# Performance work log

Hardware: AMD Instinct MI355X
Metric: run time of the kernel (lower is better)

## Reference

```python
import jax, jax.numpy as jnp
import numpy as np

N_NODES = 10000
N_EDGES = 100000
D_IN = 2 * 1280   # concat of row/col node embeddings
H1 = 512
H2 = 256


def gcn_conv(x, edge_index, W, b):
    """PyG GCNConv: add self-loops, symmetric deg^-1/2 normalization,
    x @ W then scatter-add of normalized messages, plus bias.
    num_nodes is inferred from x.shape[0] (here = n_edges, faithful to source)."""
    N = x.shape[0]
    loops = jnp.arange(N, dtype=edge_index.dtype)
    row = jnp.concatenate([edge_index[0], loops])  # sources
    col = jnp.concatenate([edge_index[1], loops])  # targets
    deg = jax.ops.segment_sum(jnp.ones_like(row, dtype=x.dtype), col, num_segments=N)
    dinv = jax.lax.rsqrt(deg)  # deg >= 1 thanks to self-loops
    norm = dinv[row] * dinv[col]  # [E+N]
    h = x @ W  # [N, out]
    out = jax.ops.segment_sum(h[row] * norm[:, None], col, num_segments=N)
    return out + b


def setup_inputs() -> dict:
    key = jax.random.key(0)
    ks = jax.random.split(key, 9)
    x = jax.random.normal(ks[0], (N_NODES, 1280), dtype=jnp.float32)
    edge_index = jax.random.randint(ks[1], (2, N_EDGES), 0, N_NODES, dtype=jnp.int32)
    # uniform noise for gumbel-sigmoid (torch.rand); keep strictly in (0,1)
    eps = jax.random.uniform(ks[2], (N_EDGES, 1), jnp.float32, 1e-6, 1.0 - 1e-6)
    W1 = jax.random.normal(ks[3], (D_IN, H1), jnp.float32) * (1.0 / np.sqrt(D_IN))
    b1 = jnp.zeros((H1,), jnp.float32)
    W2 = jax.random.normal(ks[4], (H1, H2), jnp.float32) * (1.0 / np.sqrt(H1))
    b2 = jnp.zeros((H2,), jnp.float32)
    Wl = jax.random.normal(ks[5], (H2, 1), jnp.float32) * (1.0 / np.sqrt(H2))
    bl = jnp.zeros((1,), jnp.float32)
    return {"x": x, "edge_index": edge_index, "eps": eps,
            "W1": W1, "b1": b1, "W2": W2, "b2": b2, "Wl": Wl, "bl": bl}


def reference(x, edge_index, eps, W1, b1, W2, b2, Wl, bl):
    rows, cols = edge_index[0], edge_index[1]
    # per-edge explainer input: concat of endpoint embeddings -> [E, 2560]
    input_embs = jnp.concatenate([x[rows], x[cols]], axis=1)
    h = jax.nn.relu(gcn_conv(input_embs, edge_index, W1, b1))
    h = jax.nn.relu(gcn_conv(h, edge_index, W2, b2))
    pre = h @ Wl + bl  # [E, 1] sampling weights
    # gumbel-sigmoid sampling (temperature = 1.0)
    gate = jnp.log(eps) - jnp.log1p(-eps) + pre
    mask = jax.nn.sigmoid(gate)
    pos, neg = mask, 1.0 - mask
    kld = jnp.mean(pos * jnp.log(pos / 0.5 + 1e-8) + neg * jnp.log(neg / 0.5 + 1e-9))
    return (kld, mask)
```

## Files before the change

### kernel.cpp

```cpp
#include <hip/hip_runtime.h>
#include <cstdint>
#include <cstddef>

#define H1DIM 512
#define H2DIM 256
#define DNODE 1280
#define NPACK 1024

typedef __attribute__((ext_vector_type(8))) short short8v;
typedef __attribute__((ext_vector_type(4))) float f32x4;
typedef __attribute__((ext_vector_type(4))) unsigned short us4;

__device__ __forceinline__ unsigned short f2bf(float f) {
    unsigned int u = __builtin_bit_cast(unsigned int, f);
    u += 0x7fffu + ((u >> 16) & 1u);
    return (unsigned short)(u >> 16);
}
__device__ __forceinline__ float bf2f(unsigned short h) {
    unsigned int u = ((unsigned int)h) << 16;
    return __builtin_bit_cast(float, u);
}

__device__ __forceinline__ int cmi(int R, int kq) {
    return ((R >> 4) << 9) + (((kq >> 3) << 4) + (R & 15)) * 8;
}

__global__ __launch_bounds__(256) void prep_k(
    const float* __restrict__ x, unsigned short* __restrict__ xb, int ncvt, int ntot,
    const int* __restrict__ e1, int* __restrict__ hist, int nhist, int E,
    const float* __restrict__ W1, unsigned short* __restrict__ Bpt1,
    const float* __restrict__ W2, unsigned short* __restrict__ W2t)
{
    __shared__ float tile[32][33];
    int b = blockIdx.x;

    if (b < ncvt) {
        int i = b * 256 + threadIdx.x;
        if (i * 4 < ntot) {
            f32x4 v = *reinterpret_cast<const f32x4*>(x + (size_t)i * 4);
            us4 o;
            o[0] = f2bf(v.x); o[1] = f2bf(v.y); o[2] = f2bf(v.z); o[3] = f2bf(v.w);
            *reinterpret_cast<us4*>(xb + (size_t)i * 4) = o;
        }
        return;
    }
    b -= ncvt;
    if (b < nhist) {
        int e = b * 256 + threadIdx.x;
        if (e < E) atomicAdd(&hist[e1[e]], 1);
        return;
    }
    b -= nhist;

    const float* src; unsigned short* dst; int ldsrc, lddst, bx, by;
    if (b < 640) {
        src = W1; dst = Bpt1; ldsrc = H1DIM; lddst = DNODE; bx = b & 15; by = b >> 4;
    } else if (b < 1280) {
        b -= 640;
        src = W1 + (size_t)DNODE * H1DIM; dst = Bpt1 + (size_t)H1DIM * DNODE;
        ldsrc = H1DIM; lddst = DNODE; bx = b & 15; by = b >> 4;
    } else {
        b -= 1280;
        src = W2; dst = W2t; ldsrc = H2DIM; lddst = H1DIM; bx = b & 7; by = b >> 3;
    }
    const int c0 = bx * 32, r0 = by * 32;
    const int tx = threadIdx.x & 31;
    const int ty = threadIdx.x >> 5;
#pragma unroll
    for (int rr = ty; rr < 32; rr += 8)
        tile[rr][tx] = src[(size_t)(r0 + rr) * ldsrc + c0 + tx];
    __syncthreads();
#pragma unroll
    for (int rr = ty; rr < 32; rr += 8)
        dst[(size_t)(c0 + rr) * lddst + r0 + tx] = f2bf(tile[tx][rr]);
}

template <int MODE>
__global__ __launch_bounds__(512) void gemm_u_k(
    const unsigned short* __restrict__ Ab,
    const unsigned short* __restrict__ Bt,
    unsigned short* __restrict__ Cb,
    const unsigned short* __restrict__ out1b,
    const unsigned short* __restrict__ XWb16,
    const float* __restrict__ b1,
    const float* __restrict__ b2,
    const float* __restrict__ Wl,
    const int* __restrict__ e0, const int* __restrict__ e1,
    unsigned short* __restrict__ h2b, float* __restrict__ pre_raw,
    int* __restrict__ hist, int* __restrict__ off, int* __restrict__ cursor,
    float* __restrict__ dinv,
    int M, int K, int Nn, int nwg)
{
    const int tid  = threadIdx.x;

    if (MODE == 0 && blockIdx.x >= nwg) {
        __shared__ int part[512];
        const int t = tid;
        const int per = (Nn + 511) / 512;
        const int base = t * per;
        int s = 0;
        for (int i = 0; i < per; ++i) { int b = base + i; if (b < Nn) s += hist[b]; }
        part[t] = s;
        __syncthreads();
        for (int d = 1; d < 512; d <<= 1) {
            int v = (t >= d) ? part[t - d] : 0;
            __syncthreads();
            part[t] += v;
            __syncthreads();
        }
        int run = (t == 0) ? 0 : part[t - 1];
        for (int i = 0; i < per; ++i) {
            int b = base + i;
            if (b < Nn) {
                int h = hist[b];
                off[b] = run;
                run += h;
                cursor[b] = 0;
                dinv[b] = rsqrtf(1.0f + (float)h);
            }
        }
        if (t == 511) off[Nn] = run;
        return;
    }

    __shared__ alignas(16) unsigned short As[2][128 * 32];
    __shared__ alignas(16) unsigned short Bs[2][256 * 32];
    __shared__ float b1s[H1DIM];
    __shared__ float b2s[H2DIM];
    __shared__ float wls[H2DIM];
    __shared__ float preacc[128];

    const int lane = tid & 63;
    const int w    = tid >> 6;
    const int wm   = w >> 2, wn = w & 3;

    int mb, n0;
    if (MODE == 0) {
        const int q = nwg >> 3, r = nwg & 7;
        const int xcd = blockIdx.x & 7;
        const int base = (xcd < r) ? xcd * (q + 1) : r * (q + 1) + (xcd - r) * q;
        const int wg = base + (blockIdx.x >> 3);
        mb = wg >> 2;
        n0 = (wg & 3) << 8;
    } else {
        mb = blockIdx.x;
        n0 = 0;
    }
    const int m0 = mb * 128;

    if (MODE == 1) {
        if (tid < 128) preacc[tid] = 0.f;
        if (tid < 256) { b2s[tid] = b2[tid]; wls[tid] = Wl[tid]; }
        b1s[tid] = b1[tid];
    }

    const int sa_r = tid >> 2, sa_k = (tid & 3) << 3;
    const int sb_r = tid >> 1, sb_k = (tid & 1) << 4;
    const int gma  = m0 + sa_r;
    const bool aval = (gma < M);

    const int aw  = cmi(sa_r, sa_k);
    const int bw0 = cmi(sb_r, sb_k);
    const int bw1 = cmi(sb_r, sb_k + 8);

    const unsigned short* bsrc = Bt + (size_t)(n0 + sb_r) * K + sb_k;
    const unsigned short* s1 = nullptr;
    const unsigned short* s2 = nullptr;
    bool dual = false;
    if (MODE == 0) {
        if (aval) s1 = Ab + (size_t)gma * K + sa_k;
    } else if (aval) {
        if (gma < Nn) {
            s1 = out1b + (size_t)gma * H1DIM + sa_k;
        } else {
            s1 = XWb16 + (size_t)e0[gma] * NPACK + sa_k;
            s2 = XWb16 + (size_t)e1[gma] * NPACK + H1DIM + sa_k;
            dual = true;
        }
    }
    if (MODE == 1) __syncthreads();

    f32x4 acc[4][4];
#pragma unroll
    for (int i = 0; i < 4; ++i)
#pragma unroll
        for (int j = 0; j < 4; ++j) acc[i][j] = f32x4{0.f, 0.f, 0.f, 0.f};

    short8v ab1, ab2, bb0, bb1;

    auto load_tile = [&](int k0) {
        bb0 = *reinterpret_cast<const short8v*>(bsrc + k0);
        bb1 = *reinterpret_cast<const short8v*>(bsrc + k0 + 8);
        if (aval) {
            ab1 = *reinterpret_cast<const short8v*>(s1 + k0);
            if (MODE == 1 && dual) ab2 = *reinterpret_cast<const short8v*>(s2 + k0);
        }
    };
    auto write_lds = [&](int buf, int k0) {
        *reinterpret_cast<short8v*>(&Bs[buf][bw0]) = bb0;
        *reinterpret_cast<short8v*>(&Bs[buf][bw1]) = bb1;
        short8v av;
        if (!aval) {
            av = short8v{0,0,0,0,0,0,0,0};
        } else if (MODE == 0 || !dual) {
            av = ab1;
        } else {
#pragma unroll
            for (int ii = 0; ii < 8; ++ii) {
                float v = bf2f((unsigned short)ab1[ii]) + bf2f((unsigned short)ab2[ii])
                        + b1s[k0 + sa_k + ii];
                v = fmaxf(v, 0.f);
                av[ii] = (short)f2bf(v);
            }
        }
        *reinterpret_cast<short8v*>(&As[buf][aw]) = av;
    };

    load_tile(0);
    int buf = 0;
    for (int k0 = 0; k0 < K; k0 += 32) {
        write_lds(buf, k0);
        __syncthreads();
        if (k0 + 32 < K) load_tile(k0 + 32);

        const unsigned short* ard = &As[buf][(wm * 4) * 512 + lane * 8];
        const unsigned short* brd = &Bs[buf][(wn * 4) * 512 + lane * 8];
        short8v af[4], bfq[4];
#pragma unroll
        for (int i = 0; i < 4; ++i)
            af[i] = *reinterpret_cast<const short8v*>(ard + i * 512);
#pragma unroll
        for (int j = 0; j < 4; ++j)
            bfq[j] = *reinterpret_cast<const short8v*>(brd + j * 512);
#pragma unroll
        for (int i = 0; i < 4; ++i)
#pragma unroll
            for (int j = 0; j < 4; ++j)
                acc[i][j] = __builtin_amdgcn_mfma_f32_16x16x32_bf16(af[i], bfq[j], acc[i][j], 0, 0, 0);
        buf ^= 1;
    }

    const int crow0 = m0 + wm * 64 + ((lane >> 4) << 2);
    if (MODE == 0) {
        const int ccol = n0 + wn * 64 + (lane & 15);
#pragma unroll
        for (int i = 0; i < 4; ++i)
#pragma unroll
            for (int q = 0; q < 4; ++q) {
                const int row = crow0 + i * 16 + q;
                if (row < M) {
#pragma unroll
                    for (int j = 0; j < 4; ++j)
                        Cb[(size_t)row * NPACK + ccol + j * 16] = f2bf(acc[i][j][q]);
                }
            }
    } else {
        const int cbase = wn * 64 + (lane & 15);
#pragma unroll
        for (int i = 0; i < 4; ++i)
#pragma unroll
            for (int q = 0; q < 4; ++q) {
                float v = 0.f;
#pragma unroll
                for (int j = 0; j < 4; ++j) {
                    const int c = cbase + j * 16;
                    v += fmaxf(acc[i][j][q] + b2s[c], 0.f) * wls[c];
                }
                v += __shfl_xor(v, 1, 64);
                v += __shfl_xor(v, 2, 64);
                v += __shfl_xor(v, 4, 64);
                v += __shfl_xor(v, 8, 64);
                if ((lane & 15) == 0)
                    atomicAdd(&preacc[wm * 64 + i * 16 + ((lane >> 4) << 2) + q], v);
            }
        if (m0 < Nn) {
            const int ccol = wn * 64 + (lane & 15);
#pragma unroll
            for (int i = 0; i < 4; ++i)
#pragma unroll
                for (int q = 0; q < 4; ++q) {
                    const int row = crow0 + i * 16 + q;
                    if (row < Nn) {
#pragma unroll
                        for (int j = 0; j < 4; ++j)
                            h2b[(size_t)row * H2DIM + ccol + j * 16] = f2bf(acc[i][j][q]);
                    }
                }
        }
        __syncthreads();
        if (tid < 128) {
            const int gm = m0 + tid;
            if (gm >= Nn && gm < M) pre_raw[gm] = preacc[tid];
        }
    }
}

__global__ __launch_bounds__(256) void build1_fill_k(
    const unsigned short* __restrict__ XWb16, const float* __restrict__ dinv,
    const int* __restrict__ e0, const int* __restrict__ e1,
    unsigned short* __restrict__ H1b,
    const int* __restrict__ off, int* __restrict__ cursor, int* __restrict__ srcs,
    int N, int E)
{
    int b = blockIdx.x;
    if (b < N) {
        const int a = e0[b], c = e1[b];
        const float dv = dinv[b];
        const unsigned short* pt = XWb16 + (size_t)a * NPACK;
        const unsigned short* pb = XWb16 + (size_t)c * NPACK + H1DIM;
        const int j = threadIdx.x * 2;
        const unsigned ut = *reinterpret_cast<const unsigned*>(pt + j);
        const unsigned ub = *reinterpret_cast<const unsigned*>(pb + j);
        const float ox = (bf2f((unsigned short)(ut & 0xffff)) + bf2f((unsigned short)(ub & 0xffff))) * dv;
        const float oy = (bf2f((unsigned short)(ut >> 16))   + bf2f((unsigned short)(ub >> 16)))   * dv;
        const unsigned pk = (unsigned)f2bf(ox) | ((unsigned)f2bf(oy) << 16);
        *reinterpret_cast<unsigned*>(H1b + (size_t)b * H1DIM + j) = pk;
        return;
    }
    int e = (b - N) * 256 + threadIdx.x;
    if (e < E) {
        int t = e1[e];
        int p = off[t] + atomicAdd(&cursor[t], 1);
        srcs[p] = e0[e];
    }
}

__global__ __launch_bounds__(256) void agg1_k(
    const unsigned short* __restrict__ H1b, const int* __restrict__ off, const int* __restrict__ srcs,
    const float* __restrict__ b1, const float* __restrict__ dinv,
    unsigned short* __restrict__ out1b)
{
    const int t = blockIdx.x;
    const int j = threadIdx.x * 2;
    const int s0 = off[t], s1e = off[t + 1];
    const float dt = dinv[t];
    const unsigned u0 = *reinterpret_cast<const unsigned*>(H1b + (size_t)t * H1DIM + j);
    float ax = bf2f((unsigned short)(u0 & 0xffff));
    float ay = bf2f((unsigned short)(u0 >> 16));
    for (int i = s0; i < s1e; ++i) {
        const unsigned v = *reinterpret_cast<const unsigned*>(H1b + (size_t)srcs[i] * H1DIM + j);
        ax += bf2f((unsigned short)(v & 0xffff));
        ay += bf2f((unsigned short)(v >> 16));
    }
    const float ox = fmaxf(b1[j]     + dt * ax, 0.f);
    const float oy = fmaxf(b1[j + 1] + dt * ay, 0.f);
    const unsigned pk = (unsigned)f2bf(ox) | ((unsigned)f2bf(oy) << 16);
    *reinterpret_cast<unsigned*>(out1b + (size_t)t * H1DIM + j) = pk;
}

__global__ __launch_bounds__(128) void agg2_k(
    const unsigned short* __restrict__ h2b, const int* __restrict__ off, const int* __restrict__ srcs,
    const float* __restrict__ b2, const float* __restrict__ Wl,
    const float* __restrict__ dinv, float* __restrict__ pre_low)
{
    __shared__ float part[2];
    const int t = blockIdx.x;
    const int j = threadIdx.x * 2;
    const int s0 = off[t], s1e = off[t + 1];
    const float dt = dinv[t];
    const unsigned u0 = *reinterpret_cast<const unsigned*>(h2b + (size_t)t * H2DIM + j);
    float ax = bf2f((unsigned short)(u0 & 0xffff)) * dt;
    float ay = bf2f((unsigned short)(u0 >> 16)) * dt;
    for (int i = s0; i < s1e; ++i) {
        const int s = srcs[i];
        const float ds = dinv[s];
        const unsigned v = *reinterpret_cast<const unsigned*>(h2b + (size_t)s * H2DIM + j);
        ax += bf2f((unsigned short)(v & 0xffff)) * ds;
        ay += bf2f((unsigned short)(v >> 16)) * ds;
    }
    float p = fmaxf(b2[j]     + dt * ax, 0.f) * Wl[j]
            + fmaxf(b2[j + 1] + dt * ay, 0.f) * Wl[j + 1];
#pragma unroll
    for (int o = 32; o; o >>= 1) p += __shfl_down(p, o, 64);
    if ((threadIdx.x & 63) == 0) part[threadIdx.x >> 6] = p;
    __syncthreads();
    if (threadIdx.x == 0) pre_low[t] = part[0] + part[1];
}

__global__ __launch_bounds__(256) void final2_k(
    const float* __restrict__ pre_low, const float* __restrict__ pre_raw,
    const float* __restrict__ blp, const float* __restrict__ eps,
    float* __restrict__ dout, int E, int Nn)
{
    __shared__ float part[4];
    const int i = blockIdx.x * 256 + threadIdx.x;
    float kld = 0.f;
    if (i < E) {
        const float pre = ((i < Nn) ? pre_low[i] : pre_raw[i]) + blp[0];
        const float ee = eps[i];
        const float gate = logf(ee) - log1pf(-ee) + pre;
        const float m = 1.0f / (1.0f + expf(-gate));
        dout[1 + i] = m;
        const float pos = m, neg = 1.0f - m;
        kld = pos * logf(pos * 2.0f + 1e-8f) + neg * logf(neg * 2.0f + 1e-9f);
    }
#pragma unroll
    for (int o = 32; o; o >>= 1) kld += __shfl_down(kld, o, 64);
    const int lane = threadIdx.x & 63, wv = threadIdx.x >> 6;
    if (lane == 0) part[wv] = kld;
    __syncthreads();
    if (threadIdx.x == 0)
        atomicAdd(&dout[0], (part[0] + part[1] + part[2] + part[3]) / (float)E);
}

extern "C" void kernel_launch(void* const* d_in, const int* in_sizes, int n_in,
                              void* d_out, int out_size, void* d_ws, size_t ws_size,
                              hipStream_t stream)
{
    const float* x   = (const float*)d_in[0];
    const int*   ei  = (const int*)d_in[1];
    const float* eps = (const float*)d_in[2];
    const float* W1  = (const float*)d_in[3];
    const float* b1  = (const float*)d_in[4];
    const float* W2  = (const float*)d_in[5];
    const float* b2  = (const float*)d_in[6];
    const float* Wl  = (const float*)d_in[7];
    const float* bl  = (const float*)d_in[8];
    float* out = (float*)d_out;
    float* ws  = (float*)d_ws;

    const int N = in_sizes[0] / DNODE;
    const int E = in_sizes[1] / 2;
    const int* e0 = ei;
    const int* e1 = ei + E;

    float* dinv     = ws;
    float* pre_raw  = dinv + 16384;
    float* pre_low  = pre_raw + E;
    float* fend     = pre_low + 16384;
    unsigned short* XWb16 = (unsigned short*)fend;
    unsigned short* out1b = XWb16 + (size_t)N * NPACK;
    unsigned short* H1b   = out1b + (size_t)N * H1DIM;
    unsigned short* h2b   = H1b + (size_t)N * H1DIM;
    unsigned short* xb    = h2b + (size_t)N * H2DIM;
    unsigned short* Bpt1  = xb + (size_t)N * DNODE;
    unsigned short* W2t   = Bpt1 + (size_t)NPACK * DNODE;
    int* hist   = (int*)(W2t + (size_t)H2DIM * H1DIM);
    int* cursor = hist + N;
    int* off    = cursor + N;
    int* srcs   = off + (N + 1);

    hipMemsetAsync(hist, 0, (size_t)N * sizeof(int), stream);
    hipMemsetAsync(out, 0, sizeof(float), stream);

    {
        const int ntot = N * DNODE;
        const int ncvt = (ntot / 4 + 255) / 256;
        const int nhist = (E + 255) / 256;
        const int ntr = 640 + 640 + 128;
        prep_k<<<ncvt + nhist + ntr, 256, 0, stream>>>(
            x, xb, ncvt, ntot, e1, hist, nhist, E, W1, Bpt1, W2, W2t);
    }

    {
        const int nwg = 4 * ((N + 127) / 128);
        gemm_u_k<0><<<nwg + 1, 512, 0, stream>>>(
            xb, Bpt1, XWb16, nullptr, nullptr, b1, b2, Wl, e0, e1,
            nullptr, nullptr, hist, off, cursor, dinv, N, DNODE, N, nwg);
    }

    build1_fill_k<<<N + (E + 255) / 256, 256, 0, stream>>>(
        XWb16, dinv, e0, e1, H1b, off, cursor, srcs, N, E);

    agg1_k<<<N, 256, 0, stream>>>(H1b, off, srcs, b1, dinv, out1b);

    {
        const int nwg = (E + 127) / 128;
        gemm_u_k<1><<<nwg, 512, 0, stream>>>(
            nullptr, W2t, nullptr, out1b, XWb16, b1, b2, Wl, e0, e1,
            h2b, pre_raw, nullptr, nullptr, nullptr, nullptr, E, H1DIM, N, nwg);
    }

    agg2_k<<<N, 128, 0, stream>>>(h2b, off, srcs, b2, Wl, dinv, pre_low);

    final2_k<<<(E + 255) / 256, 256, 0, stream>>>(pre_low, pre_raw, bl, eps, out, E, N);
}
```

Baseline: 193.2 us.

## Fuse layer-1 aggregation into layer-2 GEMM with flag sync and fold final epilogue

Moves the agg1 neighbour aggregation into the front of the MODE 1 GEMM launch. Aggregation blocks each handle two nodes and bump a global release counter. GEMM tiles that need aggregated node rows (m0 < N) spin on that counter, while tiles over raw edge rows run first. The gumbel-sigmoid and KLD epilogue now runs inside the GEMM for rows at or above N and inside agg2 for rows below N, which removes final2_k and the pre_raw/pre_low buffers. This cuts two launches and some intermediate traffic, but the spin-wait relies on the aggregation blocks being scheduled before the waiting blocks, and it adds one atomic per node in agg2.

```diff
diff --git a/kernel.cpp b/kernel.cpp
--- a/kernel.cpp
+++ b/kernel.cpp
@@ -80,20 +80,23 @@
     const unsigned short* __restrict__ Ab,
     const unsigned short* __restrict__ Bt,
     unsigned short* __restrict__ Cb,
-    const unsigned short* __restrict__ out1b,
+    unsigned short* __restrict__ out1b,
     const unsigned short* __restrict__ XWb16,
+    const unsigned short* __restrict__ H1b,
     const float* __restrict__ b1,
     const float* __restrict__ b2,
     const float* __restrict__ Wl,
     const int* __restrict__ e0, const int* __restrict__ e1,
-    unsigned short* __restrict__ h2b, float* __restrict__ pre_raw,
-    int* __restrict__ hist, int* __restrict__ off, int* __restrict__ cursor,
-    float* __restrict__ dinv,
+    int* __restrict__ off, const int* __restrict__ srcs,
+    unsigned short* __restrict__ h2b,
+    int* __restrict__ hist, int* __restrict__ cursor, float* __restrict__ dinv,
+    const float* __restrict__ eps, const float* __restrict__ blp, float* __restrict__ dout,
+    int* __restrict__ flag, int nagg,
     int M, int K, int Nn, int nwg)
 {
     const int tid  = threadIdx.x;
 
-    if (MODE == 0 && blockIdx.x >= nwg) {
+    if (MODE == 0 && blockIdx.x >= (unsigned)nwg) {
         __shared__ int part[512];
         const int t = tid;
         const int per = (Nn + 511) / 512;
@@ -123,12 +126,38 @@
         return;
     }
 
+    if (MODE == 1 && blockIdx.x < (unsigned)nagg) {
+        const int t = ((int)blockIdx.x << 1) + (tid >> 8);
+        const int j = (tid & 255) << 1;
+        if (t < Nn) {
+            const int s0 = off[t], s1e = off[t + 1];
+            const float dt = dinv[t];
+            const unsigned u0 = *reinterpret_cast<const unsigned*>(H1b + (size_t)t * H1DIM + j);
+            float ax = bf2f((unsigned short)(u0 & 0xffff));
+            float ay = bf2f((unsigned short)(u0 >> 16));
+            for (int i = s0; i < s1e; ++i) {
+                const unsigned v = *reinterpret_cast<const unsigned*>(H1b + (size_t)srcs[i] * H1DIM + j);
+                ax += bf2f((unsigned short)(v & 0xffff));
+                ay += bf2f((unsigned short)(v >> 16));
+            }
+            const float ox = fmaxf(b1[j]     + dt * ax, 0.f);
+            const float oy = fmaxf(b1[j + 1] + dt * ay, 0.f);
+            const unsigned pk = (unsigned)f2bf(ox) | ((unsigned)f2bf(oy) << 16);
+            *reinterpret_cast<unsigned*>(out1b + (size_t)t * H1DIM + j) = pk;
+        }
+        __syncthreads();
+        if (tid == 0)
+            __hip_atomic_fetch_add(flag, 1, __ATOMIC_RELEASE, __HIP_MEMORY_SCOPE_AGENT);
+        return;
+    }
+
     __shared__ alignas(16) unsigned short As[2][128 * 32];
     __shared__ alignas(16) unsigned short Bs[2][256 * 32];
     __shared__ float b1s[H1DIM];
     __shared__ float b2s[H2DIM];
     __shared__ float wls[H2DIM];
     __shared__ float preacc[128];
+    __shared__ float kpart[8];
 
     const int lane = tid & 63;
     const int w    = tid >> 6;
@@ -143,8 +172,18 @@
         mb = wg >> 2;
         n0 = (wg & 3) << 8;
     } else {
-        mb = blockIdx.x;
+        const int ndep = (Nn + 127) >> 7;
+        const int b = (int)blockIdx.x - nagg;
+        const int ngat = nwg - ndep;
+        mb = (b < ngat) ? (ndep + b) : (b - ngat);
         n0 = 0;
+        if (mb < ndep) {
+            if (tid == 0) {
+                while (__hip_atomic_load(flag, __ATOMIC_ACQUIRE, __HIP_MEMORY_SCOPE_AGENT) < nagg)
+                    __builtin_amdgcn_s_sleep(8);
+            }
+            __syncthreads();
+        }
     }
     const int m0 = mb * 128;
 
@@ -288,9 +327,28 @@
                 }
         }
         __syncthreads();
+        float kld = 0.f;
         if (tid < 128) {
             const int gm = m0 + tid;
-            if (gm >= Nn && gm < M) pre_raw[gm] = preacc[tid];
+            if (gm >= Nn && gm < M) {
+                const float pre = preacc[tid] + blp[0];
+                const float ee = eps[gm];
+                const float gate = logf(ee) - log1pf(-ee) + pre;
+                const float mk = 1.0f / (1.0f + expf(-gate));
+                dout[1 + gm] = mk;
+                kld = mk * logf(mk * 2.0f + 1e-8f)
+                    + (1.0f - mk) * logf((1.0f - mk) * 2.0f + 1e-9f);
+            }
+        }
+#pragma unroll
+        for (int o = 32; o; o >>= 1) kld += __shfl_down(kld, o, 64);
+        if (lane == 0) kpart[w] = kld;
+        __syncthreads();
+        if (tid == 0) {
+            float s = 0.f;
+#pragma unroll
+            for (int i = 0; i < 8; ++i) s += kpart[i];
+            if (s != 0.f) atomicAdd(&dout[0], s / (float)M);
         }
     }
 }
@@ -325,33 +383,12 @@
     }
 }
 
-__global__ __launch_bounds__(256) void agg1_k(
-    const unsigned short* __restrict__ H1b, const int* __restrict__ off, const int* __restrict__ srcs,
-    const float* __restrict__ b1, const float* __restrict__ dinv,
-    unsigned short* __restrict__ out1b)
-{
-    const int t = blockIdx.x;
-    const int j = threadIdx.x * 2;
-    const int s0 = off[t], s1e = off[t + 1];
-    const float dt = dinv[t];
-    const unsigned u0 = *reinterpret_cast<const unsigned*>(H1b + (size_t)t * H1DIM + j);
-    float ax = bf2f((unsigned short)(u0 & 0xffff));
-    float ay = bf2f((unsigned short)(u0 >> 16));
-    for (int i = s0; i < s1e; ++i) {
-        const unsigned v = *reinterpret_cast<const unsigned*>(H1b + (size_t)srcs[i] * H1DIM + j);
-        ax += bf2f((unsigned short)(v & 0xffff));
-        ay += bf2f((unsigned short)(v >> 16));
-    }
-    const float ox = fmaxf(b1[j]     + dt * ax, 0.f);
-    const float oy = fmaxf(b1[j + 1] + dt * ay, 0.f);
-    const unsigned pk = (unsigned)f2bf(ox) | ((unsigned)f2bf(oy) << 16);
-    *reinterpret_cast<unsigned*>(out1b + (size_t)t * H1DIM + j) = pk;
-}
-
 __global__ __launch_bounds__(128) void agg2_k(
     const unsigned short* __restrict__ h2b, const int* __restrict__ off, const int* __restrict__ srcs,
     const float* __restrict__ b2, const float* __restrict__ Wl,
-    const float* __restrict__ dinv, float* __restrict__ pre_low)
+    const float* __restrict__ dinv,
+    const float* __restrict__ eps, const float* __restrict__ blp,
+    float* __restrict__ dout, int Etot)
 {
     __shared__ float part[2];
     const int t = blockIdx.x;
@@ -374,33 +411,16 @@
     for (int o = 32; o; o >>= 1) p += __shfl_down(p, o, 64);
     if ((threadIdx.x & 63) == 0) part[threadIdx.x >> 6] = p;
     __syncthreads();
-    if (threadIdx.x == 0) pre_low[t] = part[0] + part[1];
-}
-
-__global__ __launch_bounds__(256) void final2_k(
-    const float* __restrict__ pre_low, const float* __restrict__ pre_raw,
-    const float* __restrict__ blp, const float* __restrict__ eps,
-    float* __restrict__ dout, int E, int Nn)
-{
-    __shared__ float part[4];
-    const int i = blockIdx.x * 256 + threadIdx.x;
-    float kld = 0.f;
-    if (i < E) {
-        const float pre = ((i < Nn) ? pre_low[i] : pre_raw[i]) + blp[0];
-        const float ee = eps[i];
+    if (threadIdx.x == 0) {
+        const float pre = part[0] + part[1] + blp[0];
+        const float ee = eps[t];
         const float gate = logf(ee) - log1pf(-ee) + pre;
-        const float m = 1.0f / (1.0f + expf(-gate));
-        dout[1 + i] = m;
-        const float pos = m, neg = 1.0f - m;
-        kld = pos * logf(pos * 2.0f + 1e-8f) + neg * logf(neg * 2.0f + 1e-9f);
-    }
-#pragma unroll
-    for (int o = 32; o; o >>= 1) kld += __shfl_down(kld, o, 64);
-    const int lane = threadIdx.x & 63, wv = threadIdx.x >> 6;
-    if (lane == 0) part[wv] = kld;
-    __syncthreads();
-    if (threadIdx.x == 0)
-        atomicAdd(&dout[0], (part[0] + part[1] + part[2] + part[3]) / (float)E);
+        const float mk = 1.0f / (1.0f + expf(-gate));
+        dout[1 + t] = mk;
+        const float kld = mk * logf(mk * 2.0f + 1e-8f)
+                        + (1.0f - mk) * logf((1.0f - mk) * 2.0f + 1e-9f);
+        atomicAdd(&dout[0], kld / (float)Etot);
+    }
 }
 
 extern "C" void kernel_launch(void* const* d_in, const int* in_sizes, int n_in,
@@ -425,9 +445,7 @@
     const int* e1 = ei + E;
 
     float* dinv     = ws;
-    float* pre_raw  = dinv + 16384;
-    float* pre_low  = pre_raw + E;
-    float* fend     = pre_low + 16384;
+    float* fend     = dinv + 16384;
     unsigned short* XWb16 = (unsigned short*)fend;
     unsigned short* out1b = XWb16 + (size_t)N * NPACK;
     unsigned short* H1b   = out1b + (size_t)N * H1DIM;
@@ -436,12 +454,13 @@
     unsigned short* Bpt1  = xb + (size_t)N * DNODE;
     unsigned short* W2t   = Bpt1 + (size_t)NPACK * DNODE;
     int* hist   = (int*)(W2t + (size_t)H2DIM * H1DIM);
-    int* cursor = hist + N;
+    int* flag   = hist + N;
+    int* cursor = flag + 1;
     int* off    = cursor + N;
     int* srcs   = off + (N + 1);
 
-    hipMemsetAsync(hist, 0, (size_t)N * sizeof(int), stream);
-    hipMemsetAsync(out, 0, sizeof(float), stream);
+    (void)hipMemsetAsync(hist, 0, (size_t)(N + 1) * sizeof(int), stream);
+    (void)hipMemsetAsync(out, 0, sizeof(float), stream);
 
     {
         const int ntot = N * DNODE;
@@ -455,23 +474,22 @@
     {
         const int nwg = 4 * ((N + 127) / 128);
         gemm_u_k<0><<<nwg + 1, 512, 0, stream>>>(
-            xb, Bpt1, XWb16, nullptr, nullptr, b1, b2, Wl, e0, e1,
-            nullptr, nullptr, hist, off, cursor, dinv, N, DNODE, N, nwg);
+            xb, Bpt1, XWb16, nullptr, nullptr, nullptr, b1, b2, Wl, e0, e1,
+            off, nullptr, nullptr, hist, cursor, dinv,
+            nullptr, nullptr, nullptr, nullptr, 0, N, DNODE, N, nwg);
     }
 
     build1_fill_k<<<N + (E + 255) / 256, 256, 0, stream>>>(
         XWb16, dinv, e0, e1, H1b, off, cursor, srcs, N, E);
 
-    agg1_k<<<N, 256, 0, stream>>>(H1b, off, srcs, b1, dinv, out1b);
-
     {
+        const int nagg = (N + 1) / 2;
         const int nwg = (E + 127) / 128;
-        gemm_u_k<1><<<nwg, 512, 0, stream>>>(
-            nullptr, W2t, nullptr, out1b, XWb16, b1, b2, Wl, e0, e1,
-            h2b, pre_raw, nullptr, nullptr, nullptr, nullptr, E, H1DIM, N, nwg);
-    }
-
-    agg2_k<<<N, 128, 0, stream>>>(h2b, off, srcs, b2, Wl, dinv, pre_low);
-
-    final2_k<<<(E + 255) / 256, 256, 0, stream>>>(pre_low, pre_raw, bl, eps, out, E, N);
-}
+        gemm_u_k<1><<<nagg + nwg, 512, 0, stream>>>(
+            nullptr, W2t, nullptr, out1b, XWb16, H1b, b1, b2, Wl, e0, e1,
+            off, srcs, h2b, nullptr, nullptr, dinv,
+            eps, bl, out, flag, nagg, E, H1DIM, N, nwg);
+    }
+
+    agg2_k<<<N, 128, 0, stream>>>(h2b, off, srcs, b2, Wl, dinv, eps, bl, out, E);
+}
```

New measurement: 431.3 us. 123% more time.
